# Kernel tuning notes

Measured on AMD Instinct MI355X. Metric: run time of the kernel, lower is better.

Reference implementation:

```python
import jax, jax.numpy as jnp
import numpy as np

D_MODEL = 1024
N_HEADS = 16
D_K = D_MODEL // N_HEADS
D_FF = 4096
B, S = 2, 2048
EPS = 1e-5


def setup_inputs() -> dict:
    key = jax.random.key(0)
    ks = jax.random.split(key, 16)
    sc = 0.02
    inp = {
        'x': jax.random.normal(ks[0], (B, S, D_MODEL), dtype=jnp.float32),
        'mask': jnp.ones((B, 1, 1, S), dtype=jnp.int32),
        'Wq': jax.random.normal(ks[1], (D_MODEL, D_MODEL), dtype=jnp.float32) * sc,
        'bq': jnp.zeros((D_MODEL,), dtype=jnp.float32),
        'Wk': jax.random.normal(ks[2], (D_MODEL, D_MODEL), dtype=jnp.float32) * sc,
        'bk': jnp.zeros((D_MODEL,), dtype=jnp.float32),
        'Wv': jax.random.normal(ks[3], (D_MODEL, D_MODEL), dtype=jnp.float32) * sc,
        'bv': jnp.zeros((D_MODEL,), dtype=jnp.float32),
        'Wo': jax.random.normal(ks[4], (D_MODEL, D_MODEL), dtype=jnp.float32) * sc,
        'bo': jnp.zeros((D_MODEL,), dtype=jnp.float32),
        'W1': jax.random.normal(ks[5], (D_MODEL, D_FF), dtype=jnp.float32) * sc,
        'b1': jnp.zeros((D_FF,), dtype=jnp.float32),
        'W2': jax.random.normal(ks[6], (D_FF, D_MODEL), dtype=jnp.float32) * sc,
        'b2': jnp.zeros((D_MODEL,), dtype=jnp.float32),
        'g1': jnp.ones((D_MODEL,), dtype=jnp.float32),
        'be1': jnp.zeros((D_MODEL,), dtype=jnp.float32),
        'g2': jnp.ones((D_MODEL,), dtype=jnp.float32),
        'be2': jnp.zeros((D_MODEL,), dtype=jnp.float32),
    }
    return inp


def _layernorm(x, g, b):
    mu = jnp.mean(x, axis=-1, keepdims=True)
    var = jnp.mean(jnp.square(x - mu), axis=-1, keepdims=True)
    return (x - mu) * jax.lax.rsqrt(var + EPS) * g + b


def _split_heads(x):
    b, s, _ = x.shape
    return x.reshape(b, s, N_HEADS, D_K).transpose(0, 2, 1, 3)  # [B,H,S,Dk]


def reference(x, mask, Wq, bq, Wk, bk, Wv, bv, Wo, bo, W1, b1, W2, b2, g1, be1, g2, be2):
    Q = _split_heads(x @ Wq + bq)
    K = _split_heads(x @ Wk + bk)
    V = _split_heads(x @ Wv + bv)
    scores = jnp.einsum('bhqd,bhkd->bhqk', Q, K) / jnp.sqrt(jnp.float32(D_K))
    scores = jnp.where(mask == 0, -jnp.inf, scores)
    attn = jax.nn.softmax(scores, axis=-1)
    ctx = jnp.einsum('bhqk,bhkd->bhqd', attn, V)
    ctx = ctx.transpose(0, 2, 1, 3).reshape(x.shape[0], x.shape[1], D_MODEL)
    attn_out = ctx @ Wo + bo
    h = _layernorm(x + attn_out, g1, be1)
    ff = jax.nn.relu(h @ W1 + b1) @ W2 + b2
    return _layernorm(h + ff, g2, be2)
```

## Files before the change

kernel.cpp:

```cpp
#include <hip/hip_runtime.h>
#include <hip/hip_bf16.h>

#define D_MODELC 1024
#define D_FFC    4096
#define N_HEADSC 16
#define BATCHC   2
#define SEQC     2048
#define M_TOK    (BATCHC*SEQC)

typedef __attribute__((ext_vector_type(4)))  float f32x4;
typedef __attribute__((ext_vector_type(16))) float f32x16;
typedef __attribute__((ext_vector_type(8)))  short s16x8;
using bf16_t = __hip_bfloat16;

static __device__ __forceinline__ unsigned short f2bf_u16(float f) {
  bf16_t h = __float2bfloat16(f);
  return __builtin_bit_cast(unsigned short, h);
}

static __device__ __forceinline__ unsigned int cvt_pk_bf16(float lo, float hi2) {
  unsigned int r;
  asm("v_cvt_pk_bf16_f32 %0, %1, %2" : "=v"(r) : "v"(lo), "v"(hi2));
  return r;
}

#define PSWAP(a, b) asm volatile("v_permlane32_swap_b32 %0, %1" : "+v"(a), "+v"(b))

#define ASYNC_COPY16(dst_lds, src_g) \
  __builtin_amdgcn_global_load_lds((const __attribute__((address_space(1))) void*)(src_g), \
                                   (__attribute__((address_space(3))) void*)(dst_lds), 16, 0, 0)

__global__ __launch_bounds__(256) void k_prep(
    const float* __restrict__ x,
    const float* __restrict__ Wq, const float* __restrict__ Wk,
    const float* __restrict__ Wv, const float* __restrict__ Wo,
    const float* __restrict__ W1, const float* __restrict__ W2,
    const float* __restrict__ bq, const float* __restrict__ bk,
    const float* __restrict__ bv,
    bf16_t* __restrict__ x16, bf16_t* __restrict__ wqkvT, bf16_t* __restrict__ woT,
    bf16_t* __restrict__ w1T, bf16_t* __restrict__ w2T, float* __restrict__ bqkv) {
  __shared__ float tile[32][33];
  const int bidx = blockIdx.x;
  const int tid = threadIdx.x;

  if (bidx < 12288) {
    const float* in;
    bf16_t* out;
    int R, C, bx, by;
    if (bidx < 4096) {
      const int z = bidx >> 10, t = bidx & 1023;
      in = (z == 0) ? Wq : (z == 1) ? Wk : (z == 2) ? Wv : Wo;
      out = (z == 0) ? wqkvT : (z == 1) ? wqkvT + 1024 * 1024
           : (z == 2) ? wqkvT + 2 * 1024 * 1024 : woT;
      R = 1024; C = 1024; bx = t & 31; by = t >> 5;
    } else if (bidx < 8192) {
      const int t = bidx - 4096;
      in = W1; out = w1T; R = 1024; C = 4096; bx = t & 127; by = t >> 7;
    } else {
      const int t = bidx - 8192;
      in = W2; out = w2T; R = 4096; C = 1024; bx = t & 31; by = t >> 5;
    }
    const int tx = tid & 31, ty = tid >> 5;
    const int c0 = bx * 32, r0 = by * 32;
#pragma unroll
    for (int i = 0; i < 4; ++i)
      tile[ty + i * 8][tx] = in[(size_t)(r0 + ty + i * 8) * C + c0 + tx];
    __syncthreads();
#pragma unroll
    for (int i = 0; i < 4; ++i)
      out[(size_t)(c0 + ty + i * 8) * R + r0 + tx] = __float2bfloat16(tile[tx][ty + i * 8]);
  } else if (bidx < 16384) {
    const int i = (bidx - 12288) * 256 + tid;
    float4 v = ((const float4*)x)[i];
    short4 o;
    o.x = (short)f2bf_u16(v.x);
    o.y = (short)f2bf_u16(v.y);
    o.z = (short)f2bf_u16(v.z);
    o.w = (short)f2bf_u16(v.w);
    ((short4*)x16)[i] = o;
  } else {
    const int i = (bidx - 16384) * 256 + tid;
    float v = (i < 1024) ? bq[i] : (i < 2048) ? bk[i - 1024] : bv[i - 2048];
    bqkv[i] = v;
  }
}

__global__ __launch_bounds__(512, 2) void k_gemm256(
    const bf16_t* __restrict__ A, const bf16_t* __restrict__ BT,
    const float* __restrict__ bias, bf16_t* __restrict__ Cout,
    int N, int K, int lda, int ldb, int ldc, int mode) {
  __shared__ __align__(16) bf16_t Ab[2][256][64];
  __shared__ __align__(16) bf16_t Bb[2][256][64];

  const int nbn = N / 256;
  const int nwg = gridDim.x;
  const int cpx = nwg >> 3;
  const int wg = (blockIdx.x & 7) * cpx + (blockIdx.x >> 3);
  const int mb = wg / nbn, nb = wg % nbn;
  const int row0 = mb * 256, col0 = nb * 256;

  const int tid = threadIdx.x;
  const int w = tid >> 6, lane = tid & 63;
  const int lr = lane & 15, lg = lane >> 4;
  const int wr = w >> 2, wc = w & 3;
  const int s7 = lr & 7;

#define STAGE256(buf, kt_)                                                            \
  {                                                                                   \
    const int k0_ = (kt_) * 64;                                                       \
    _Pragma("unroll")                                                                 \
    for (int i_ = 0; i_ < 4; ++i_) {                                                  \
      int c_ = tid + i_ * 512;                                                        \
      int row_ = c_ >> 3, sg_ = (c_ & 7) ^ (row_ & 7);                                \
      ASYNC_COPY16(&Ab[buf][0][0] + (size_t)c_ * 8,                                   \
                   A + (size_t)(row0 + row_) * lda + k0_ + sg_ * 8);                  \
    }                                                                                 \
    _Pragma("unroll")                                                                 \
    for (int i_ = 0; i_ < 4; ++i_) {                                                  \
      int c_ = tid + i_ * 512;                                                        \
      int row_ = c_ >> 3, sg_ = (c_ & 7) ^ (row_ & 7);                                \
      ASYNC_COPY16(&Bb[buf][0][0] + (size_t)c_ * 8,                                   \
                   BT + (size_t)(col0 + row_) * ldb + k0_ + sg_ * 8);                 \
    }                                                                                 \
  }

  f32x4 acc[8][4];
#pragma unroll
  for (int m = 0; m < 8; ++m)
#pragma unroll
    for (int n = 0; n < 4; ++n) acc[m][n] = (f32x4){0.f, 0.f, 0.f, 0.f};

  const int nt = K / 64;
  STAGE256(0, 0)
  STAGE256(1, 1)
  asm volatile("s_waitcnt vmcnt(8)" ::: "memory");
  __builtin_amdgcn_sched_barrier(0);
  __builtin_amdgcn_s_barrier();

  for (int t = 0; t < nt; ++t) {
    const int cur = t & 1;
    s16x8 a0[8], b0[4];
#pragma unroll
    for (int m = 0; m < 8; ++m)
      a0[m] = *(const s16x8*)(&Ab[cur][wr * 128 + m * 16 + lr][(lg ^ s7) * 8]);
#pragma unroll
    for (int n = 0; n < 4; ++n)
      b0[n] = *(const s16x8*)(&Bb[cur][wc * 64 + n * 16 + lr][(lg ^ s7) * 8]);
    __builtin_amdgcn_s_setprio(1);
#pragma unroll
    for (int m = 0; m < 8; ++m)
#pragma unroll
      for (int n = 0; n < 4; ++n)
        acc[m][n] = __builtin_amdgcn_mfma_f32_16x16x32_bf16(a0[m], b0[n], acc[m][n], 0, 0, 0);
    __builtin_amdgcn_s_setprio(0);
    s16x8 a1[8], b1[4];
#pragma unroll
    for (int m = 0; m < 8; ++m)
      a1[m] = *(const s16x8*)(&Ab[cur][wr * 128 + m * 16 + lr][((4 + lg) ^ s7) * 8]);
#pragma unroll
    for (int n = 0; n < 4; ++n)
      b1[n] = *(const s16x8*)(&Bb[cur][wc * 64 + n * 16 + lr][((4 + lg) ^ s7) * 8]);
    asm volatile("s_waitcnt lgkmcnt(0)" ::: "memory");
    __builtin_amdgcn_sched_barrier(0);
    __builtin_amdgcn_s_barrier();
    if (t + 2 < nt) STAGE256(cur, t + 2)
    __builtin_amdgcn_s_setprio(1);
#pragma unroll
    for (int m = 0; m < 8; ++m)
#pragma unroll
      for (int n = 0; n < 4; ++n)
        acc[m][n] = __builtin_amdgcn_mfma_f32_16x16x32_bf16(a1[m], b1[n], acc[m][n], 0, 0, 0);
    __builtin_amdgcn_s_setprio(0);
    if (t + 2 < nt) {
      asm volatile("s_waitcnt vmcnt(8)" ::: "memory");
    } else {
      asm volatile("s_waitcnt vmcnt(0)" ::: "memory");
    }
    __builtin_amdgcn_sched_barrier(0);
    __builtin_amdgcn_s_barrier();
  }

#pragma unroll
  for (int m = 0; m < 8; ++m) {
    int grow = row0 + wr * 128 + m * 16 + lg * 4;
#pragma unroll
    for (int n = 0; n < 4; ++n) {
      int gcol = col0 + wc * 64 + n * 16 + lr;
      float bv = bias[gcol];
      float cs = (mode == 3 && gcol < 1024) ? 0.18033688f : 1.f;
#pragma unroll
      for (int r = 0; r < 4; ++r) {
        float v = (acc[m][n][r] + bv) * cs;
        if (mode == 1) v = fmaxf(v, 0.f);
        Cout[(size_t)(grow + r) * ldc + gcol] = __float2bfloat16(v);
      }
    }
  }
#undef STAGE256
}

#define GBK 64

__global__ __launch_bounds__(256, 2) void k_gemm(
    const bf16_t* __restrict__ A, const bf16_t* __restrict__ BT,
    const float* __restrict__ bias,
    float* __restrict__ p0, float* __restrict__ p1,
    void* __restrict__ Cout, int M, int N, int K,
    int lda, int ldb, int ldc, int mode, int nsplit) {
  __shared__ __align__(16) bf16_t Asm[128 * GBK];
  __shared__ __align__(16) bf16_t Bsm[128 * GBK];

  const int nbn = N / 128;
  const int nwg = gridDim.x;
  const int cpx = nwg >> 3;
  int wg = (blockIdx.x & 7) * cpx + (blockIdx.x >> 3);
  int kslice = 0;
  if (nsplit == 2) { kslice = wg & 1; wg >>= 1; }
  const int mb = wg / nbn, nb = wg % nbn;
  const int row0 = mb * 128, col0 = nb * 128;
  A  += (size_t)kslice * K;
  BT += (size_t)kslice * K;

  const int tid = threadIdx.x;
  const int w = tid >> 6, lane = tid & 63;
  const int lr = lane & 15, lg = lane >> 4;
  const int wr = w >> 1, wc = w & 1;
  const int wbase = tid & 192;

  f32x4 acc[4][4];
#pragma unroll
  for (int m = 0; m < 4; ++m)
#pragma unroll
    for (int n = 0; n < 4; ++n) acc[m][n] = (f32x4){0.f, 0.f, 0.f, 0.f};

  for (int k0 = 0; k0 < K; k0 += GBK) {
    __syncthreads();
#pragma unroll
    for (int i = 0; i < 4; ++i) {
      int c = i * 256 + tid;
      int row = c >> 3;
      int sg = (c & 7) ^ (row & 7);
      ASYNC_COPY16(Asm + (size_t)(i * 256 + wbase) * 8,
                   A + (size_t)(row0 + row) * lda + k0 + sg * 8);
    }
#pragma unroll
    for (int i = 0; i < 4; ++i) {
      int c = i * 256 + tid;
      int row = c >> 3;
      int sg = (c & 7) ^ (row & 7);
      ASYNC_COPY16(Bsm + (size_t)(i * 256 + wbase) * 8,
                   BT + (size_t)(col0 + row) * ldb + k0 + sg * 8);
    }
    __syncthreads();
#pragma unroll
    for (int kst = 0; kst < 2; ++kst) {
      const int sl = ((kst * 4 + lg) ^ (lr & 7)) * 8;
      s16x8 af[4], bfr[4];
#pragma unroll
      for (int m = 0; m < 4; ++m)
        af[m] = *(const s16x8*)(Asm + (size_t)(wr * 64 + m * 16 + lr) * GBK + sl);
#pragma unroll
      for (int n = 0; n < 4; ++n)
        bfr[n] = *(const s16x8*)(Bsm + (size_t)(wc * 64 + n * 16 + lr) * GBK + sl);
#pragma unroll
      for (int m = 0; m < 4; ++m)
#pragma unroll
        for (int n = 0; n < 4; ++n)
          acc[m][n] = __builtin_amdgcn_mfma_f32_16x16x32_bf16(af[m], bfr[n], acc[m][n], 0, 0, 0);
    }
  }

  float* outf = (kslice == 0) ? p0 : p1;
  bf16_t* outh = (bf16_t*)Cout;
#pragma unroll
  for (int m = 0; m < 4; ++m) {
    int grow = row0 + wr * 64 + m * 16 + lg * 4;
#pragma unroll
    for (int n = 0; n < 4; ++n) {
      int gcol = col0 + wc * 64 + n * 16 + lr;
      float bv = (mode == 4) ? 0.f : bias[gcol];
#pragma unroll
      for (int r = 0; r < 4; ++r) {
        float v = acc[m][n][r] + bv;
        size_t idx = (size_t)(grow + r) * ldc + gcol;
        if (mode == 4) {
          outf[idx] = v;
        } else {
          if (mode == 1) v = fmaxf(v, 0.f);
          outh[idx] = __float2bfloat16(v);
        }
      }
    }
  }
}

__global__ __launch_bounds__(256, 4) void k_attn(
    const bf16_t* __restrict__ qkv, const int* __restrict__ mask,
    bf16_t* __restrict__ pA, bf16_t* __restrict__ pB,
    float* __restrict__ psA, float* __restrict__ psB) {
  const int bid = blockIdx.x;
  const int j = (bid & 7) + ((bid >> 7) << 3);
  const int qt = (bid >> 3) & 15;
  const int h = j & 15;
  const int b = (j >> 4) & 1;
  const int half = j >> 5;
  const int tid = threadIdx.x;
  const int w = tid >> 6, lane = tid & 63;
  const int l31 = lane & 31, hi = lane >> 5;
  const int wbase = tid & 192;

  __shared__ __align__(16) bf16_t Kl[2][64][64];
  __shared__ __align__(16) bf16_t Vl[2][4096];

  const int tokb = b * SEQC;
  const int q0 = qt * 128 + w * 32;
  const int kb0 = half * (SEQC / 2);

  s16x8 qfrag[4];
  {
    const bf16_t* qp = qkv + (size_t)(tokb + q0 + l31) * 3072 + h * 64 + hi * 8;
#pragma unroll
    for (int s = 0; s < 4; ++s) qfrag[s] = *(const s16x8*)(qp + s * 16);
  }

  char* klc = (char*)&Kl[0][0][0];
  bf16_t* Vl0 = &Vl[0][0];
  const unsigned vbase =
      (unsigned)(size_t)(__attribute__((address_space(3))) bf16_t*)Vl0 + lane * 8;

  int vkey0, vd0, vkey1, vd1;
  {
    int c = tid, L = c >> 3;
    int f_ = L >> 4, t_ = (L >> 3) & 1, db_ = (L >> 2) & 1, h_ = (L >> 1) & 1, dl_ = L & 1;
    vkey0 = 16 * f_ + 8 * h_ + 4 * t_ + ((c & 7) >> 1);
    vd0 = ((db_ * 2 + dl_) << 4) + (c & 1) * 8;
  }
  {
    int c = tid + 256, L = c >> 3;
    int f_ = L >> 4, t_ = (L >> 3) & 1, db_ = (L >> 2) & 1, h_ = (L >> 1) & 1, dl_ = L & 1;
    vkey1 = 16 * f_ + 8 * h_ + 4 * t_ + ((c & 7) >> 1);
    vd1 = ((db_ * 2 + dl_) << 4) + (c & 1) * 8;
  }
  const bf16_t* srcV0 = qkv + (size_t)(tokb + kb0 + vkey0) * 3072 + 2048 + (size_t)h * 64 + vd0;
  const bf16_t* srcV1 = qkv + (size_t)(tokb + kb0 + vkey1) * 3072 + 2048 + (size_t)h * 64 + vd1;
  const int krow0 = ((w * 2 + 0) * 8) + (lane >> 3);
  const int krow1 = ((w * 2 + 1) * 8) + (lane >> 3);
  const bf16_t* srcK0 = qkv + (size_t)(tokb + kb0 + krow0) * 3072 + 1024 + (size_t)h * 64
                        + (((lane & 7) ^ (krow0 & 7)) * 8);
  const bf16_t* srcK1 = qkv + (size_t)(tokb + kb0 + krow1) * 3072 + 1024 + (size_t)h * 64
                        + (((lane & 7) ^ (krow1 & 7)) * 8);
  const int* mptr = mask + tokb + kb0 + lane;

#define STAGE_K(buf)                                                                  \
  {                                                                                   \
    ASYNC_COPY16(&Kl[buf][(w * 2 + 0) * 8][0], srcK0);                                \
    ASYNC_COPY16(&Kl[buf][(w * 2 + 1) * 8][0], srcK1);                                \
    srcK0 += 64 * 3072;                                                               \
    srcK1 += 64 * 3072;                                                               \
  }

#define STAGE_V(buf)                                                                  \
  {                                                                                   \
    ASYNC_COPY16(Vl0 + (size_t)(buf) * 4096 + (size_t)wbase * 8, srcV0);              \
    ASYNC_COPY16(Vl0 + (size_t)(buf) * 4096 + (size_t)(256 + wbase) * 8, srcV1);      \
    srcV0 += 64 * 3072;                                                               \
    srcV1 += 64 * 3072;                                                               \
  }

  float mreg_cur, mreg_nxt;
  bool allv_cur, allv_nxt;
  {
    mreg_cur = (*mptr) ? 1.f : 0.f;
    mptr += 64;
    unsigned long long z = __ballot(mreg_cur == 0.f);
    allv_cur = (z == 0ull);
  }

  STAGE_K(0)
  STAGE_V(0)

  f32x16 o[2];
#pragma unroll
  for (int d = 0; d < 2; ++d)
#pragma unroll
    for (int i = 0; i < 16; ++i) o[d][i] = 0.f;
  float psum = 0.f;

  __syncthreads();

  for (int kt = 0; kt < SEQC / 128; ++kt) {
    const int cur = kt & 1, nxt = cur ^ 1;
    const bool more = (kt < SEQC / 128 - 1);

    if (more) {
      STAGE_K(nxt)
      STAGE_V(nxt)
      mreg_nxt = (*mptr) ? 1.f : 0.f;
      mptr += 64;
      unsigned long long z = __ballot(mreg_nxt == 0.f);
      allv_nxt = (z == 0ull);
    }

    f32x16 st[2];
#pragma unroll
    for (int kk = 0; kk < 2; ++kk)
#pragma unroll
      for (int i = 0; i < 16; ++i) st[kk][i] = 0.f;
    __builtin_amdgcn_s_setprio(1);
#pragma unroll
    for (int step = 0; step < 4; ++step) {
#pragma unroll
      for (int kb2 = 0; kb2 < 2; ++kb2) {
        int key = kb2 * 32 + l31;
        int seg = (2 * step + hi) ^ (lane & 7);
        s16x8 kf = *(const s16x8*)(klc + cur * 8192 + key * 128 + seg * 16);
        st[kb2] = __builtin_amdgcn_mfma_f32_32x32x16_bf16(kf, qfrag[step], st[kb2], 0, 0, 0);
      }
    }
    __builtin_amdgcn_s_setprio(0);

    s16x8 pf[4];
#pragma unroll
    for (int kb2 = 0; kb2 < 2; ++kb2) {
      float pa[16];
      if (allv_cur) {
#pragma unroll
        for (int i = 0; i < 16; ++i) {
          float e = __builtin_exp2f(st[kb2][i]);
          pa[i] = e;
          psum += e;
        }
      } else {
#pragma unroll
        for (int g = 0; g < 4; ++g)
#pragma unroll
          for (int rr = 0; rr < 4; ++rr) {
            float mmv = __shfl(mreg_cur, rr + 8 * g + 4 * hi + 32 * kb2);
            float e = __builtin_exp2f(st[kb2][g * 4 + rr]) * mmv;
            pa[g * 4 + rr] = e;
            psum += e;
          }
      }
      unsigned int wv[8];
#pragma unroll
      for (int u = 0; u < 8; ++u) wv[u] = cvt_pk_bf16(pa[2 * u], pa[2 * u + 1]);
      unsigned int a0 = wv[0], b0 = wv[2]; PSWAP(a0, b0);
      unsigned int a1 = wv[1], b1 = wv[3]; PSWAP(a1, b1);
      unsigned int a2 = wv[4], b2 = wv[6]; PSWAP(a2, b2);
      unsigned int a3 = wv[5], b3 = wv[7]; PSWAP(a3, b3);
      uint4 u0 = {a0, a1, b0, b1};
      uint4 u1 = {a2, a3, b2, b3};
      pf[kb2 * 2 + 0] = __builtin_bit_cast(s16x8, u0);
      pf[kb2 * 2 + 1] = __builtin_bit_cast(s16x8, u1);
    }

    const unsigned va = vbase + cur * 8192;
#pragma unroll
    for (int db = 0; db < 2; ++db) {
      ulong tr[4][2];
#pragma unroll
      for (int f = 0; f < 4; ++f)
        asm volatile("ds_read_b64_tr_b16 %0, %2 offset:%c3\n\t"
                     "ds_read_b64_tr_b16 %1, %2 offset:%c4"
                     : "=v"(tr[f][0]), "=v"(tr[f][1])
                     : "v"(va), "i"((f * 16 + db * 4) * 128), "i"((f * 16 + 8 + db * 4) * 128));
      asm volatile("s_waitcnt lgkmcnt(0)" ::: "memory");
      __builtin_amdgcn_sched_barrier(0);
      __builtin_amdgcn_s_setprio(1);
#pragma unroll
      for (int f = 0; f < 4; ++f) {
        ulong2 uv = {tr[f][0], tr[f][1]};
        s16x8 vfr = __builtin_bit_cast(s16x8, uv);
        o[db] = __builtin_amdgcn_mfma_f32_32x32x16_bf16(pf[f], vfr, o[db], 0, 0, 0);
      }
      __builtin_amdgcn_s_setprio(0);
    }

    if (more) {
      mreg_cur = mreg_nxt;
      allv_cur = allv_nxt;
    }
    __syncthreads();
  }

  psum += __shfl_xor(psum, 32);
  bf16_t* po = half ? pB : pA;
  float* ps = half ? psB : psA;
#pragma unroll
  for (int dblk = 0; dblk < 2; ++dblk)
#pragma unroll
    for (int r = 0; r < 16; ++r) {
      int qq = (r & 3) + 8 * (r >> 2) + 4 * hi;
      int tok = tokb + q0 + qq;
      po[(size_t)tok * 1024 + h * 64 + dblk * 32 + l31] = __float2bfloat16(o[dblk][r]);
    }
  if (hi == 0)
    ps[(size_t)(tokb + q0 + l31) * 16 + h] = psum;
#undef STAGE_K
#undef STAGE_V
}

__global__ __launch_bounds__(256) void k_attn_merge(
    const bf16_t* __restrict__ pA, const bf16_t* __restrict__ pB,
    const float* __restrict__ psA, const float* __restrict__ psB,
    bf16_t* __restrict__ ctx) {
  const int row = blockIdx.x, tid = threadIdx.x;
  const size_t base = (size_t)row * 1024;
  const short4 a4 = ((const short4*)(pA + base))[tid];
  const short4 b4 = ((const short4*)(pB + base))[tid];
  const int hh = tid >> 4;
  const float rs = psA[row * 16 + hh] + psB[row * 16 + hh];
  const float inv = 1.f / rs;
  const bf16_t* ae = (const bf16_t*)&a4;
  const bf16_t* be = (const bf16_t*)&b4;
  short4 ob;
  short* oe = (short*)&ob;
#pragma unroll
  for (int i = 0; i < 4; ++i)
    oe[i] = (short)f2bf_u16((__bfloat162float(ae[i]) + __bfloat162float(be[i])) * inv);
  ((short4*)(ctx + base))[tid] = ob;
}

__global__ __launch_bounds__(256) void k_ln_res2(
    const float* __restrict__ p0, const float* __restrict__ p1,
    const float* __restrict__ res, const float* __restrict__ bias,
    const float* __restrict__ g, const float* __restrict__ be,
    float* __restrict__ outf, bf16_t* __restrict__ outh) {
  const int row = blockIdx.x, tid = threadIdx.x;
  const size_t base = (size_t)row * D_MODELC;
  const float4 a  = ((const float4*)(p0 + base))[tid];
  const float4 bq = ((const float4*)(p1 + base))[tid];
  const float4 c  = ((const float4*)(res + base))[tid];
  const float4 bi = ((const float4*)bias)[tid];
  float4 v;
  v.x = a.x + bq.x + c.x + bi.x;
  v.y = a.y + bq.y + c.y + bi.y;
  v.z = a.z + bq.z + c.z + bi.z;
  v.w = a.w + bq.w + c.w + bi.w;
  float s1 = v.x + v.y + v.z + v.w;
  float s2 = v.x * v.x + v.y * v.y + v.z * v.z + v.w * v.w;
#pragma unroll
  for (int mm = 1; mm < 64; mm <<= 1) {
    s1 += __shfl_xor(s1, mm);
    s2 += __shfl_xor(s2, mm);
  }
  __shared__ float sa[4], sb[4];
  const int wv = tid >> 6;
  if ((tid & 63) == 0) { sa[wv] = s1; sb[wv] = s2; }
  __syncthreads();
  s1 = sa[0] + sa[1] + sa[2] + sa[3];
  s2 = sb[0] + sb[1] + sb[2] + sb[3];
  const float mu = s1 * (1.f / D_MODELC);
  const float var = s2 * (1.f / D_MODELC) - mu * mu;
  const float rsq = rsqrtf(var + 1e-5f);
  const float4 gg = ((const float4*)g)[tid];
  const float4 bb = ((const float4*)be)[tid];
  float4 oo;
  oo.x = (v.x - mu) * rsq * gg.x + bb.x;
  oo.y = (v.y - mu) * rsq * gg.y + bb.y;
  oo.z = (v.z - mu) * rsq * gg.z + bb.z;
  oo.w = (v.w - mu) * rsq * gg.w + bb.w;
  ((float4*)(outf + base))[tid] = oo;
  if (outh) {
    short4 ob;
    ob.x = (short)f2bf_u16(oo.x);
    ob.y = (short)f2bf_u16(oo.y);
    ob.z = (short)f2bf_u16(oo.z);
    ob.w = (short)f2bf_u16(oo.w);
    ((short4*)(outh + base))[tid] = ob;
  }
}

extern "C" void kernel_launch(void* const* d_in, const int* in_sizes, int n_in,
                              void* d_out, int out_size, void* d_ws, size_t ws_size,
                              hipStream_t stream) {
  (void)in_sizes; (void)n_in; (void)out_size; (void)ws_size;
  const float* x   = (const float*)d_in[0];
  const int* mask  = (const int*)d_in[1];
  const float* Wq  = (const float*)d_in[2];
  const float* bq  = (const float*)d_in[3];
  const float* Wk  = (const float*)d_in[4];
  const float* bk  = (const float*)d_in[5];
  const float* Wv  = (const float*)d_in[6];
  const float* bv  = (const float*)d_in[7];
  const float* Wo  = (const float*)d_in[8];
  const float* bo  = (const float*)d_in[9];
  const float* W1  = (const float*)d_in[10];
  const float* b1  = (const float*)d_in[11];
  const float* W2  = (const float*)d_in[12];
  const float* b2  = (const float*)d_in[13];
  const float* g1  = (const float*)d_in[14];
  const float* be1 = (const float*)d_in[15];
  const float* g2  = (const float*)d_in[16];
  const float* be2 = (const float*)d_in[17];

  char* ws = (char*)d_ws;
  const size_t D = D_MODELC, F = D_FFC, M = M_TOK;
  const size_t SZ_X16  = M * D * 2;
  const size_t SZ_QKV  = M * 3 * D * 2;
  bf16_t* x16   = (bf16_t*)ws;
  bf16_t* ff1   = (bf16_t*)ws;
  bf16_t* qkvb  = (bf16_t*)(ws + SZ_X16);
  size_t off = SZ_X16 + SZ_QKV;
  bf16_t* ctx   = (bf16_t*)(ws + off); off += M * D * 2;
  bf16_t* wqkvT = (bf16_t*)(ws + off); off += 3 * D * D * 2;
  bf16_t* woT   = (bf16_t*)(ws + off); off += D * D * 2;
  bf16_t* w1T   = (bf16_t*)(ws + off); off += D * F * 2;
  bf16_t* w2T   = (bf16_t*)(ws + off); off += D * F * 2;
  float*  partA = (float*)(ws + off);  off += M * D * 4;
  float*  hbuf  = (float*)(ws + off);  off += M * D * 4;
  bf16_t* h16   = (bf16_t*)(ws + off); off += M * D * 2;
  float*  partB = (float*)(ws + off);  off += M * D * 4;
  float*  bqkv  = (float*)(ws + off);  off += 3 * D * 4;
  float*  psA   = (float*)(ws + off);  off += M * 16 * 4;
  float*  psB   = (float*)(ws + off);  off += M * 16 * 4;

  k_prep<<<16396, 256, 0, stream>>>(x, Wq, Wk, Wv, Wo, W1, W2, bq, bk, bv,
                                    x16, wqkvT, woT, w1T, w2T, bqkv);

  k_gemm256<<<192, 512, 0, stream>>>(x16, wqkvT, bqkv, qkvb,
                                     3072, 1024, 1024, 1024, 3072, 3);

  k_attn<<<1024, 256, 0, stream>>>(qkvb, mask, (bf16_t*)partA, (bf16_t*)partB, psA, psB);
  k_attn_merge<<<4096, 256, 0, stream>>>((bf16_t*)partA, (bf16_t*)partB, psA, psB, ctx);

  k_gemm<<<512, 256, 0, stream>>>(ctx, woT, nullptr, partA, partB, nullptr,
                                  4096, 1024, 512, 1024, 1024, 1024, 4, 2);
  k_ln_res2<<<4096, 256, 0, stream>>>(partA, partB, x, bo, g1, be1, hbuf, h16);

  k_gemm256<<<256, 512, 0, stream>>>(h16, w1T, b1, ff1,
                                     4096, 1024, 1024, 1024, 4096, 1);
  k_gemm<<<512, 256, 0, stream>>>(ff1, w2T, nullptr, partA, partB, nullptr,
                                  4096, 1024, 2048, 4096, 4096, 1024, 4, 2);
  k_ln_res2<<<4096, 256, 0, stream>>>(partA, partB, hbuf, b2, g2, be2, (float*)d_out, nullptr);
}
```

Before: 230.6 us.

## Use 256-tile GEMM with 4-way split-K and bf16 partials for Wo/FFN2

Replaces the 128x128 split-K=2 GEMM used for the output projection and second FFN matmul with the pipelined 256x256 GEMM kernel, now extended to support a 4-way K split. Each slice writes bf16 partial sums into four contiguous buffers, and a new layernorm kernel sums the four partials with the residual and bias. The aim is to reuse the faster double-buffered large-tile kernel and to halve partial-sum traffic by storing bf16 instead of fp32. The cost is reduced precision in the partial sums from bf16 rounding, and the larger tiles only give 256 workgroups.

Result: slower. 237.7 us (+3.1%).

```diff
diff --git a/kernel.cpp b/kernel.cpp
--- a/kernel.cpp
+++ b/kernel.cpp
@@ -88,16 +88,22 @@
 __global__ __launch_bounds__(512, 2) void k_gemm256(
     const bf16_t* __restrict__ A, const bf16_t* __restrict__ BT,
     const float* __restrict__ bias, bf16_t* __restrict__ Cout,
-    int N, int K, int lda, int ldb, int ldc, int mode) {
+    int N, int K, int lda, int ldb, int ldc, int mode, int nsplit, size_t sliceStride) {
   __shared__ __align__(16) bf16_t Ab[2][256][64];
   __shared__ __align__(16) bf16_t Bb[2][256][64];
 
   const int nbn = N / 256;
   const int nwg = gridDim.x;
   const int cpx = nwg >> 3;
-  const int wg = (blockIdx.x & 7) * cpx + (blockIdx.x >> 3);
+  int wg = (blockIdx.x & 7) * cpx + (blockIdx.x >> 3);
+  int kslice = 0;
+  if (nsplit == 4) { kslice = wg & 3; wg >>= 2; }
+  const int Ks = K / nsplit;
   const int mb = wg / nbn, nb = wg % nbn;
   const int row0 = mb * 256, col0 = nb * 256;
+  A  += (size_t)kslice * Ks;
+  BT += (size_t)kslice * Ks;
+  bf16_t* Cbase = (mode == 5) ? (Cout + (size_t)kslice * sliceStride) : Cout;
 
   const int tid = threadIdx.x;
   const int w = tid >> 6, lane = tid & 63;
@@ -130,7 +136,7 @@
 #pragma unroll
     for (int n = 0; n < 4; ++n) acc[m][n] = (f32x4){0.f, 0.f, 0.f, 0.f};
 
-  const int nt = K / 64;
+  const int nt = Ks / 64;
   STAGE256(0, 0)
   STAGE256(1, 1)
   asm volatile("s_waitcnt vmcnt(8)" ::: "memory");
@@ -186,112 +192,17 @@
 #pragma unroll
     for (int n = 0; n < 4; ++n) {
       int gcol = col0 + wc * 64 + n * 16 + lr;
-      float bv = bias[gcol];
+      float bv = (mode == 5) ? 0.f : bias[gcol];
       float cs = (mode == 3 && gcol < 1024) ? 0.18033688f : 1.f;
 #pragma unroll
       for (int r = 0; r < 4; ++r) {
         float v = (acc[m][n][r] + bv) * cs;
         if (mode == 1) v = fmaxf(v, 0.f);
-        Cout[(size_t)(grow + r) * ldc + gcol] = __float2bfloat16(v);
+        Cbase[(size_t)(grow + r) * ldc + gcol] = __float2bfloat16(v);
       }
     }
   }
 #undef STAGE256
-}
-
-#define GBK 64
-
-__global__ __launch_bounds__(256, 2) void k_gemm(
-    const bf16_t* __restrict__ A, const bf16_t* __restrict__ BT,
-    const float* __restrict__ bias,
-    float* __restrict__ p0, float* __restrict__ p1,
-    void* __restrict__ Cout, int M, int N, int K,
-    int lda, int ldb, int ldc, int mode, int nsplit) {
-  __shared__ __align__(16) bf16_t Asm[128 * GBK];
-  __shared__ __align__(16) bf16_t Bsm[128 * GBK];
-
-  const int nbn = N / 128;
-  const int nwg = gridDim.x;
-  const int cpx = nwg >> 3;
-  int wg = (blockIdx.x & 7) * cpx + (blockIdx.x >> 3);
-  int kslice = 0;
-  if (nsplit == 2) { kslice = wg & 1; wg >>= 1; }
-  const int mb = wg / nbn, nb = wg % nbn;
-  const int row0 = mb * 128, col0 = nb * 128;
-  A  += (size_t)kslice * K;
-  BT += (size_t)kslice * K;
-
-  const int tid = threadIdx.x;
-  const int w = tid >> 6, lane = tid & 63;
-  const int lr = lane & 15, lg = lane >> 4;
-  const int wr = w >> 1, wc = w & 1;
-  const int wbase = tid & 192;
-
-  f32x4 acc[4][4];
-#pragma unroll
-  for (int m = 0; m < 4; ++m)
-#pragma unroll
-    for (int n = 0; n < 4; ++n) acc[m][n] = (f32x4){0.f, 0.f, 0.f, 0.f};
-
-  for (int k0 = 0; k0 < K; k0 += GBK) {
-    __syncthreads();
-#pragma unroll
-    for (int i = 0; i < 4; ++i) {
-      int c = i * 256 + tid;
-      int row = c >> 3;
-      int sg = (c & 7) ^ (row & 7);
-      ASYNC_COPY16(Asm + (size_t)(i * 256 + wbase) * 8,
-                   A + (size_t)(row0 + row) * lda + k0 + sg * 8);
-    }
-#pragma unroll
-    for (int i = 0; i < 4; ++i) {
-      int c = i * 256 + tid;
-      int row = c >> 3;
-      int sg = (c & 7) ^ (row & 7);
-      ASYNC_COPY16(Bsm + (size_t)(i * 256 + wbase) * 8,
-                   BT + (size_t)(col0 + row) * ldb + k0 + sg * 8);
-    }
-    __syncthreads();
-#pragma unroll
-    for (int kst = 0; kst < 2; ++kst) {
-      const int sl = ((kst * 4 + lg) ^ (lr & 7)) * 8;
-      s16x8 af[4], bfr[4];
-#pragma unroll
-      for (int m = 0; m < 4; ++m)
-        af[m] = *(const s16x8*)(Asm + (size_t)(wr * 64 + m * 16 + lr) * GBK + sl);
-#pragma unroll
-      for (int n = 0; n < 4; ++n)
-        bfr[n] = *(const s16x8*)(Bsm + (size_t)(wc * 64 + n * 16 + lr) * GBK + sl);
-#pragma unroll
-      for (int m = 0; m < 4; ++m)
-#pragma unroll
-        for (int n = 0; n < 4; ++n)
-          acc[m][n] = __builtin_amdgcn_mfma_f32_16x16x32_bf16(af[m], bfr[n], acc[m][n], 0, 0, 0);
-    }
-  }
-
-  float* outf = (kslice == 0) ? p0 : p1;
-  bf16_t* outh = (bf16_t*)Cout;
-#pragma unroll
-  for (int m = 0; m < 4; ++m) {
-    int grow = row0 + wr * 64 + m * 16 + lg * 4;
-#pragma unroll
-    for (int n = 0; n < 4; ++n) {
-      int gcol = col0 + wc * 64 + n * 16 + lr;
-      float bv = (mode == 4) ? 0.f : bias[gcol];
-#pragma unroll
-      for (int r = 0; r < 4; ++r) {
-        float v = acc[m][n][r] + bv;
-        size_t idx = (size_t)(grow + r) * ldc + gcol;
-        if (mode == 4) {
-          outf[idx] = v;
-        } else {
-          if (mode == 1) v = fmaxf(v, 0.f);
-          outh[idx] = __float2bfloat16(v);
-        }
-      }
-    }
-  }
 }
 
 __global__ __launch_bounds__(256, 4) void k_attn(
@@ -521,22 +432,26 @@
   ((short4*)(ctx + base))[tid] = ob;
 }
 
-__global__ __launch_bounds__(256) void k_ln_res2(
-    const float* __restrict__ p0, const float* __restrict__ p1,
+__global__ __launch_bounds__(256) void k_ln_res4(
+    const bf16_t* __restrict__ p, size_t stride,
     const float* __restrict__ res, const float* __restrict__ bias,
     const float* __restrict__ g, const float* __restrict__ be,
     float* __restrict__ outf, bf16_t* __restrict__ outh) {
   const int row = blockIdx.x, tid = threadIdx.x;
   const size_t base = (size_t)row * D_MODELC;
-  const float4 a  = ((const float4*)(p0 + base))[tid];
-  const float4 bq = ((const float4*)(p1 + base))[tid];
+  float4 v;
   const float4 c  = ((const float4*)(res + base))[tid];
   const float4 bi = ((const float4*)bias)[tid];
-  float4 v;
-  v.x = a.x + bq.x + c.x + bi.x;
-  v.y = a.y + bq.y + c.y + bi.y;
-  v.z = a.z + bq.z + c.z + bi.z;
-  v.w = a.w + bq.w + c.w + bi.w;
+  v.x = c.x + bi.x; v.y = c.y + bi.y; v.z = c.z + bi.z; v.w = c.w + bi.w;
+#pragma unroll
+  for (int s = 0; s < 4; ++s) {
+    const short4 q4 = ((const short4*)(p + s * stride + base))[tid];
+    const bf16_t* qe = (const bf16_t*)&q4;
+    v.x += __bfloat162float(qe[0]);
+    v.y += __bfloat162float(qe[1]);
+    v.z += __bfloat162float(qe[2]);
+    v.w += __bfloat162float(qe[3]);
+  }
   float s1 = v.x + v.y + v.z + v.w;
   float s2 = v.x * v.x + v.y * v.y + v.z * v.z + v.w * v.w;
 #pragma unroll
@@ -608,9 +523,10 @@
   bf16_t* w1T   = (bf16_t*)(ws + off); off += D * F * 2;
   bf16_t* w2T   = (bf16_t*)(ws + off); off += D * F * 2;
   float*  partA = (float*)(ws + off);  off += M * D * 4;
+  float*  partB = (float*)(ws + off);  off += M * D * 4;
+  bf16_t* pquad = (bf16_t*)partA;
   float*  hbuf  = (float*)(ws + off);  off += M * D * 4;
   bf16_t* h16   = (bf16_t*)(ws + off); off += M * D * 2;
-  float*  partB = (float*)(ws + off);  off += M * D * 4;
   float*  bqkv  = (float*)(ws + off);  off += 3 * D * 4;
   float*  psA   = (float*)(ws + off);  off += M * 16 * 4;
   float*  psB   = (float*)(ws + off);  off += M * 16 * 4;
@@ -619,18 +535,18 @@
                                     x16, wqkvT, woT, w1T, w2T, bqkv);
 
   k_gemm256<<<192, 512, 0, stream>>>(x16, wqkvT, bqkv, qkvb,
-                                     3072, 1024, 1024, 1024, 3072, 3);
+                                     3072, 1024, 1024, 1024, 3072, 3, 1, 0);
 
   k_attn<<<1024, 256, 0, stream>>>(qkvb, mask, (bf16_t*)partA, (bf16_t*)partB, psA, psB);
   k_attn_merge<<<4096, 256, 0, stream>>>((bf16_t*)partA, (bf16_t*)partB, psA, psB, ctx);
 
-  k_gemm<<<512, 256, 0, stream>>>(ctx, woT, nullptr, partA, partB, nullptr,
-                                  4096, 1024, 512, 1024, 1024, 1024, 4, 2);
-  k_ln_res2<<<4096, 256, 0, stream>>>(partA, partB, x, bo, g1, be1, hbuf, h16);
+  k_gemm256<<<256, 512, 0, stream>>>(ctx, woT, nullptr, pquad,
+                                     1024, 1024, 1024, 1024, 1024, 5, 4, M * D);
+  k_ln_res4<<<4096, 256, 0, stream>>>(pquad, M * D, x, bo, g1, be1, hbuf, h16);
 
   k_gemm256<<<256, 512, 0, stream>>>(h16, w1T, b1, ff1,
-                                     4096, 1024, 1024, 1024, 4096, 1);
-  k_gemm<<<512, 256, 0, stream>>>(ff1, w2T, nullptr, partA, partB, nullptr,
-                                  4096, 1024, 2048, 4096, 4096, 1024, 4, 2);
-  k_ln_res2<<<4096, 256, 0, stream>>>(partA, partB, hbuf, b2, g2, be2, (float*)d_out, nullptr);
-}
+                                     4096, 1024, 1024, 1024, 4096, 1, 1, 0);
+  k_gemm256<<<256, 512, 0, stream>>>(ff1, w2T, nullptr, pquad,
+                                     1024, 4096, 4096, 4096, 1024, 5, 4, M * D);
+  k_ln_res4<<<4096, 256, 0, stream>>>(pquad, M * D, hbuf, b2, g2, be2, (float*)d_out, nullptr);
+}
```
